# Optimization experiments

Hardware: AMD Instinct MI355X
Metric: run time of the kernel (lower is better)

The kernel has to match this reference:

```python
import jax, jax.numpy as jnp
import numpy as np

N_HEADS = 32
N_KV_HEADS = 8
HEAD_DIM = 128
DIM = 4096
BSZ = 2
SEQLEN = 2048
ROPE_THETA = 500000.0


def setup_inputs() -> dict:
    key = jax.random.key(0)
    ks = jax.random.split(key, 6)
    s = 0.02
    x = jax.random.normal(ks[0], (BSZ, SEQLEN, DIM), dtype=jnp.float32)
    wq = jax.random.normal(ks[1], (N_HEADS * HEAD_DIM, DIM), dtype=jnp.float32) * s
    wk = jax.random.normal(ks[2], (N_KV_HEADS * HEAD_DIM, DIM), dtype=jnp.float32) * s
    wv = jax.random.normal(ks[3], (N_KV_HEADS * HEAD_DIM, DIM), dtype=jnp.float32) * s
    wo = jax.random.normal(ks[4], (DIM, N_HEADS * HEAD_DIM), dtype=jnp.float32) * s
    cache_k = jnp.zeros((BSZ, SEQLEN, N_KV_HEADS, HEAD_DIM), dtype=jnp.float32)
    cache_v = jnp.zeros((BSZ, SEQLEN, N_KV_HEADS, HEAD_DIM), dtype=jnp.float32)
    # rotary frequencies: freqs_cis[t, j] = exp(i * t * theta^(-2j/hd)); pass cos/sin parts
    inv = 1.0 / (ROPE_THETA ** (jnp.arange(0, HEAD_DIM, 2, dtype=jnp.float32) / HEAD_DIM))
    t = jnp.arange(SEQLEN, dtype=jnp.float32)
    ang = jnp.outer(t, inv)  # [S, hd/2]
    freqs_cos = jnp.cos(ang)
    freqs_sin = jnp.sin(ang)
    # causal additive mask
    mask = jnp.triu(jnp.full((SEQLEN, SEQLEN), -jnp.inf, dtype=jnp.float32), k=1)
    return {"x": x, "wq": wq, "wk": wk, "wv": wv, "wo": wo,
            "cache_k": cache_k, "cache_v": cache_v,
            "freqs_cos": freqs_cos, "freqs_sin": freqs_sin,
            "mask": mask, "start_pos": 0}


def _apply_rope(t, cos, sin):
    # t: [B, S, h, hd]; cos/sin: [S, hd/2]
    B, S, h, hd = t.shape
    tf = t.astype(jnp.float32).reshape(B, S, h, hd // 2, 2)
    a, b = tf[..., 0], tf[..., 1]
    c = cos[None, :, None, :]
    s = sin[None, :, None, :]
    out = jnp.stack([a * c - b * s, a * s + b * c], axis=-1)
    return out.reshape(B, S, h, hd).astype(t.dtype)


def reference(x, wq, wk, wv, wo, cache_k, cache_v, freqs_cos, freqs_sin, mask, start_pos):
    B, S, D = x.shape
    hd = HEAD_DIM
    n_rep = N_HEADS // N_KV_HEADS
    xq = (x @ wq.T).reshape(B, S, N_HEADS, hd)
    xk = (x @ wk.T).reshape(B, S, N_KV_HEADS, hd)
    xv = (x @ wv.T).reshape(B, S, N_KV_HEADS, hd)
    xq = _apply_rope(xq, freqs_cos, freqs_sin)
    xk = _apply_rope(xk, freqs_cos, freqs_sin)
    # KV cache write + slice
    cache_k = jax.lax.dynamic_update_slice(cache_k, xk, (0, start_pos, 0, 0))
    cache_v = jax.lax.dynamic_update_slice(cache_v, xv, (0, start_pos, 0, 0))
    kv_len = start_pos + S
    keys = cache_k[:B, :kv_len]    # [B, K, kvh, hd]
    values = cache_v[:B, :kv_len]
    # GQA: repeat kv heads
    keys = jnp.repeat(keys, n_rep, axis=2)     # [B, K, H, hd]
    values = jnp.repeat(values, n_rep, axis=2)
    q = xq.transpose(0, 2, 1, 3)       # [B, H, S, hd]
    k = keys.transpose(0, 2, 1, 3)     # [B, H, K, hd]
    v = values.transpose(0, 2, 1, 3)
    scores = jnp.einsum('bhqd,bhkd->bhqk', q, k) / jnp.sqrt(jnp.float32(hd))
    if mask is not None:
        scores = scores + mask[None, None, :, :]
    probs = jax.nn.softmax(scores.astype(jnp.float32), axis=-1).astype(q.dtype)
    out = jnp.einsum('bhqk,bhkd->bhqd', probs, v)
    out = out.transpose(0, 2, 1, 3).reshape(B, S, N_HEADS * hd)
    return out @ wo.T
```

## Files before the change

### kernel.cpp

```cpp
#include <hip/hip_runtime.h>
#include <hip/hip_bf16.h>
#include <math.h>

typedef __attribute__((ext_vector_type(8)))  __bf16 bfrag;
typedef __attribute__((ext_vector_type(4)))  float  f32x4;
typedef __attribute__((ext_vector_type(16))) float  f32x16;
typedef __attribute__((ext_vector_type(8)))  short  s16x8;
typedef __attribute__((ext_vector_type(4)))  short  s16x4;
typedef __attribute__((ext_vector_type(2)))  unsigned u32x2;
typedef __attribute__((ext_vector_type(4)))  unsigned u32x4;

__device__ __forceinline__ short f2bf(float f) {
  return (short)__builtin_bit_cast(unsigned short, (__bf16)f);
}
__device__ __forceinline__ float bf2f(short s) {
  return (float)__builtin_bit_cast(__bf16, (unsigned short)s);
}
__device__ __forceinline__ unsigned cvtpk(float lo, float hi_) {
  unsigned r;
  asm("v_cvt_pk_bf16_f32 %0, %1, %2" : "=v"(r) : "v"(lo), "v"(hi_));
  return r;
}
__device__ __forceinline__ void gll16(const void* g, void* l) {
  __builtin_amdgcn_global_load_lds((const __attribute__((address_space(1))) void*)g,
                                   (__attribute__((address_space(3))) void*)l, 16, 0, 0);
}

__global__ __launch_bounds__(256) void cvt_f32_bf16(const float* __restrict__ in,
                                                    short* __restrict__ out, int n4) {
  int i = blockIdx.x * 256 + threadIdx.x;
  if (i >= n4) return;
  f32x4 v = ((const f32x4*)in)[i];
  s16x4 o;
  o.x = f2bf(v.x); o.y = f2bf(v.y); o.z = f2bf(v.z); o.w = f2bf(v.w);
  ((s16x4*)out)[i] = o;
}

__global__ __launch_bounds__(256) void cvt4(const float* __restrict__ x,
                                            const float* __restrict__ wq,
                                            const float* __restrict__ wk,
                                            const float* __restrict__ wv,
                                            short* __restrict__ xb,
                                            short* __restrict__ wqb,
                                            short* __restrict__ wkb,
                                            short* __restrict__ wvb) {
  const int b = blockIdx.x;
  const float* in; short* out; int base;
  if (b < 16384)      { in = x;  out = xb;  base = 0; }
  else if (b < 32768) { in = wq; out = wqb; base = 16384 * 256; }
  else if (b < 36864) { in = wk; out = wkb; base = 32768 * 256; }
  else                { in = wv; out = wvb; base = 36864 * 256; }
  const int idx = b * 256 + threadIdx.x - base;
  f32x4 v = ((const f32x4*)in)[idx];
  s16x4 o;
  o.x = f2bf(v.x); o.y = f2bf(v.y); o.z = f2bf(v.z); o.w = f2bf(v.w);
  ((s16x4*)out)[idx] = o;
}

template<bool BF16OUT>
__global__ __launch_bounds__(512) void gemm128n(const short* __restrict__ A,
                                                const short* __restrict__ B,
                                                void* __restrict__ Cv,
                                                int M, int N, int K, int NBX) {
  __shared__ __align__(16) short As[2][128 * 64];
  __shared__ __align__(16) short Bs[2][256 * 64];
  const int tid = threadIdx.x, lane = tid & 63, wid = tid >> 6;
  const int lr = lane & 15, lg = lane >> 4;
  const int wm = wid >> 2, wn = wid & 3;
  const int orig = blockIdx.x;
  const int xc = orig & 7, o8 = orig >> 3;
  const int s8 = o8 >> 5, t8 = o8 & 31;
  const int bmi = ((xc >> 1) << 3) + (t8 >> 2);
  const int bni = (xc & 1) * (NBX >> 1) + (s8 << 2) + (t8 & 3);
  const int bm = bmi << 7, bn = bni << 8;
  const int NT = K >> 6;
  const int r0 = tid >> 3;
  const int c0 = tid & 7;
  const int csrc = c0 ^ (r0 & 7);

#define STG(OP, OPs, boff, bb, hh, kt_)                                          \
  do {                                                                           \
    _Pragma("unroll")                                                            \
    for (int s = 0; s < 2; ++s)                                                  \
      gll16(OP + (size_t)(boff + (hh) * 128 + s * 64 + r0) * K + (kt_) * 64 + csrc * 8, \
            (char*)OPs[bb] + ((hh) * 128 + s * 64 + wid * 8) * 128);             \
  } while (0)

  int ch[2];
#pragma unroll
  for (int ks = 0; ks < 2; ++ks) ch[ks] = (((ks << 2) | lg) ^ (lr & 7)) << 4;
  const int aoff  = (wm * 64 + lr) * 128;
  const int boff2 = (wn * 32 + lr) * 128;

#define RD_A(dst, bb)                                                            \
  do {                                                                           \
    const char* ab = (const char*)As[bb] + aoff;                                 \
    _Pragma("unroll") for (int i = 0; i < 4; ++i)                                \
      _Pragma("unroll") for (int ks = 0; ks < 2; ++ks)                           \
        dst[i][ks] = *(const bfrag*)(ab + i * 2048 + ch[ks]);                    \
  } while (0)
#define RD_B(dst, bb, jh)                                                        \
  do {                                                                           \
    const char* bp = (const char*)Bs[bb] + boff2 + (jh) * 16384;                 \
    _Pragma("unroll") for (int j = 0; j < 2; ++j)                                \
      _Pragma("unroll") for (int ks = 0; ks < 2; ++ks)                           \
        dst[j][ks] = *(const bfrag*)(bp + j * 2048 + ch[ks]);                    \
  } while (0)
#define MFMA16(af, bf, jh)                                                       \
  do {                                                                           \
    __builtin_amdgcn_s_setprio(1);                                               \
    _Pragma("unroll") for (int ks = 0; ks < 2; ++ks)                             \
      _Pragma("unroll") for (int i = 0; i < 4; ++i)                              \
        _Pragma("unroll") for (int j = 0; j < 2; ++j)                            \
          acc[i][(jh) * 2 + j] = __builtin_amdgcn_mfma_f32_16x16x32_bf16(        \
              af[i][ks], bf[j][ks], acc[i][(jh) * 2 + j], 0, 0, 0);              \
    __builtin_amdgcn_s_setprio(0);                                               \
  } while (0)

  STG(A, As, bm, 0, 0, 0);
  STG(B, Bs, bn, 0, 0, 0);
  STG(B, Bs, bn, 0, 1, 0);
  if (NT > 1) {
    STG(A, As, bm, 1, 0, 1);
    STG(B, Bs, bn, 1, 0, 1);
    asm volatile("s_waitcnt vmcnt(4)" ::: "memory");
  } else {
    asm volatile("s_waitcnt vmcnt(0)" ::: "memory");
  }
  __builtin_amdgcn_s_barrier();
  __builtin_amdgcn_sched_barrier(0);

  f32x4 acc[4][4] = {};
  bfrag a_[4][2], b_lo[2][2], b_hi[2][2];

  for (int kt = 0; kt < NT; ++kt) {
    const int b = kt & 1;
    RD_A(a_, b);
    RD_B(b_lo, b, 0);
    if (kt + 1 < NT) STG(B, Bs, bn, b ^ 1, 1, kt + 1);
    MFMA16(a_, b_lo, 0);
    __builtin_amdgcn_s_barrier();
    __builtin_amdgcn_sched_barrier(0);
    RD_B(b_hi, b, 1);
    if (kt + 2 < NT) {
      STG(A, As, bm, b, 0, kt + 2);
      STG(B, Bs, bn, b, 0, kt + 2);
    }
    MFMA16(a_, b_hi, 1);
    if (kt + 1 < NT) {
      if (kt + 2 < NT) asm volatile("s_waitcnt vmcnt(4)" ::: "memory");
      else             asm volatile("s_waitcnt vmcnt(0)" ::: "memory");
      __builtin_amdgcn_s_barrier();
      __builtin_amdgcn_sched_barrier(0);
    }
  }
#undef STG
#undef RD_A
#undef RD_B
#undef MFMA16
  const int rb = bm + wm * 64 + lg * 4, cb = bn + wn * 32 + lr;
#pragma unroll
  for (int i = 0; i < 4; ++i)
#pragma unroll
    for (int jh = 0; jh < 2; ++jh)
#pragma unroll
      for (int j = 0; j < 2; ++j)
#pragma unroll
        for (int r = 0; r < 4; ++r) {
          size_t idx = (size_t)(rb + i * 16 + r) * N + (cb + jh * 128 + j * 16);
          if (BF16OUT) ((short*)Cv)[idx] = f2bf(acc[i][jh * 2 + j][r]);
          else         ((float*)Cv)[idx] = acc[i][jh * 2 + j][r];
        }
}

__global__ __launch_bounds__(256) void rope_k(short* __restrict__ qkv,
                                              const float* __restrict__ fcos,
                                              const float* __restrict__ fsin) {
  const int t = blockIdx.x;
  const int s = t & 2047;
  unsigned* row = (unsigned*)(qkv + (size_t)t * 6144);
  for (int p = threadIdx.x; p < 2560; p += 256) {
    const int h = p >> 6, i = p & 63;
    const int w = h * 64 + i;
    unsigned u = row[w];
    float a  = bf2f((short)(u & 0xffff));
    float b  = bf2f((short)(u >> 16));
    float c  = fcos[s * 64 + i], sn = fsin[s * 64 + i];
    float na = a * c - b * sn;
    float nb = a * sn + b * c;
    row[w] = ((unsigned)(unsigned short)f2bf(na)) |
             (((unsigned)(unsigned short)f2bf(nb)) << 16);
  }
}

__global__ __launch_bounds__(256) void vtrans(const short* __restrict__ qkv,
                                              short* __restrict__ vt) {
  const int sb = blockIdx.x, kvh = blockIdx.y, b = blockIdx.z;
  __shared__ short T[64][136];
  const int tid = threadIdx.x;
#pragma unroll
  for (int it = 0; it < 4; ++it) {
    int c = it * 256 + tid;
    int r = c >> 4, dc = c & 15;
    s16x8 v = *(const s16x8*)(qkv + (size_t)(b * 2048 + sb * 64 + r) * 6144
                              + 5120 + kvh * 128 + dc * 8);
    *(s16x8*)&T[r][dc * 8] = v;
  }
  __syncthreads();
#pragma unroll
  for (int it = 0; it < 4; ++it) {
    int c = it * 256 + tid;
    int d = c >> 3, sc = c & 7;
    s16x8 v;
#pragma unroll
    for (int j = 0; j < 8; ++j) v[j] = T[sc * 8 + j][d];
    *(s16x8*)(vt + (size_t)((b * 8 + kvh) * 128 + d) * 2048 + sb * 64 + sc * 8) = v;
  }
}

__global__ __launch_bounds__(512, 2) void fattn2(const short* __restrict__ qkv,
                                                 const short* __restrict__ vt,
                                                 short* __restrict__ ao) {
  const int b = blockIdx.z, h = blockIdx.y;
  const int qb = b ? (int)gridDim.x - 1 - blockIdx.x : blockIdx.x;
  const int kvh = h >> 2;
  const int tid = threadIdx.x;
  const int lane = tid & 63, wid = tid >> 6;
  const int l31 = lane & 31, hi = lane >> 5;
  __shared__ __align__(16) short Ks[2][64 * 128];
  __shared__ __align__(16) short Vs[2][128 * 64];

  const int q0w   = qb * 256 + wid * 32;
  const int qg    = q0w + l31;
  const int tmaxw = q0w >> 6;
  const int NT    = 4 * qb + 4;

  bfrag qf[8];
  {
    const short* qp = qkv + (size_t)(b * 2048 + qg) * 6144 + h * 128 + hi * 8;
#pragma unroll
    for (int kk = 0; kk < 8; ++kk) qf[kk] = *(const bfrag*)(qp + kk * 16);
  }

  const int kr0 = tid >> 4, kcc = tid & 15;
  const int vd0 = tid >> 3, vkc = tid & 7;
  const int kro[2] = { kr0, kr0 + 32 };
  const int vdo[2] = { vd0, vd0 + 64 };
  int kldst[2], vldst[2];
#pragma unroll
  for (int i = 0; i < 2; ++i) {
    kldst[i] = (kro[i] * 256 + kcc * 16) ^ ((kro[i] & 7) << 4);
    vldst[i] = (vdo[i] * 128 + vkc * 16) ^ ((vdo[i] & 7) << 4);
  }
  const short* base_k = qkv + (size_t)(b * 2048) * 6144 + 4096 + kvh * 128;
  const short* base_v = vt + (size_t)((b * 8 + kvh) * 128) * 2048;

  {
    s16x8 kr_[2], vr_[2];
#pragma unroll
    for (int i = 0; i < 2; ++i) {
      kr_[i] = *(const s16x8*)(base_k + (size_t)kro[i] * 6144 + kcc * 8);
      vr_[i] = *(const s16x8*)(base_v + (size_t)vdo[i] * 2048 + vkc * 8);
    }
#pragma unroll
    for (int i = 0; i < 2; ++i) {
      *(s16x8*)((char*)Ks[0] + kldst[i]) = kr_[i];
      *(s16x8*)((char*)Vs[0] + vldst[i]) = vr_[i];
    }
  }
  __syncthreads();

  f32x16 o[4] = {};
  float m = -3.0e38f, l = 0.f;
  const float c0 = 0.08838834764831845f * 1.4426950408889634f;
  const int  sw = (l31 & 7) << 4;

  for (int t = 0; t < NT; ++t) {
    const int cur = t & 1;
    s16x8 kr_[2], vr_[2];
    const bool pf = (t + 1 < NT);
    if (pf) {
#pragma unroll
      for (int i = 0; i < 2; ++i) {
        kr_[i] = *(const s16x8*)(base_k + (size_t)((t + 1) * 64 + kro[i]) * 6144 + kcc * 8);
        vr_[i] = *(const s16x8*)(base_v + (size_t)vdo[i] * 2048 + (t + 1) * 64 + vkc * 8);
      }
    }
    if (t <= tmaxw) {
      f32x16 st[2] = {};
      {
        const char* kb = (const char*)Ks[cur] + l31 * 256;
        __builtin_amdgcn_s_setprio(1);
#pragma unroll
        for (int kk = 0; kk < 8; ++kk) {
          const int ko = (kk * 32 + hi * 16) ^ sw;
          bfrag kf0 = *(const bfrag*)(kb + ko);
          bfrag kf1 = *(const bfrag*)(kb + 8192 + ko);
          st[0] = __builtin_amdgcn_mfma_f32_32x32x16_bf16(kf0, qf[kk], st[0], 0, 0, 0);
          st[1] = __builtin_amdgcn_mfma_f32_32x32x16_bf16(kf1, qf[kk], st[1], 0, 0, 0);
        }
        __builtin_amdgcn_s_setprio(0);
      }
      if (t == tmaxw) {
        const int kb0 = t * 64 + 4 * hi;
#pragma unroll
        for (int kt = 0; kt < 2; ++kt)
#pragma unroll
          for (int r = 0; r < 16; ++r) {
            int k = kb0 + kt * 32 + (r & 3) + 8 * (r >> 2);
            if (k > qg) st[kt][r] = -3.0e38f;
          }
      }
      float mt = -3.0e38f;
#pragma unroll
      for (int kt = 0; kt < 2; ++kt)
#pragma unroll
        for (int r = 0; r < 16; ++r) mt = fmaxf(mt, st[kt][r]);
      mt = fmaxf(mt, __shfl_xor(mt, 32, 64));
      if (!__all((mt - m) * c0 <= 8.0f)) {
        float nm = fmaxf(m, mt);
        float fe = exp2f((m - nm) * c0);
        m = nm;
        l *= fe;
#pragma unroll
        for (int dt = 0; dt < 4; ++dt)
#pragma unroll
          for (int r = 0; r < 16; ++r) o[dt][r] *= fe;
      }
      const float mc = m * c0;
      float ps = 0.f;
#pragma unroll
      for (int kt = 0; kt < 2; ++kt)
#pragma unroll
        for (int r = 0; r < 16; ++r) {
          float p = exp2f(st[kt][r] * c0 - mc);
          st[kt][r] = p;
          ps += p;
        }
      ps += __shfl_xor(ps, 32, 64);
      l += ps;
      bfrag pfr[4];
#pragma unroll
      for (int kt = 0; kt < 2; ++kt) {
        u32x2 a0 = __builtin_amdgcn_permlane32_swap(cvtpk(st[kt][0],  st[kt][1]),
                                                    cvtpk(st[kt][4],  st[kt][5]),  0, 0);
        u32x2 a1 = __builtin_amdgcn_permlane32_swap(cvtpk(st[kt][2],  st[kt][3]),
                                                    cvtpk(st[kt][6],  st[kt][7]),  0, 0);
        u32x2 b0 = __builtin_amdgcn_permlane32_swap(cvtpk(st[kt][8],  st[kt][9]),
                                                    cvtpk(st[kt][12], st[kt][13]), 0, 0);
        u32x2 b1 = __builtin_amdgcn_permlane32_swap(cvtpk(st[kt][10], st[kt][11]),
                                                    cvtpk(st[kt][14], st[kt][15]), 0, 0);
        u32x4 w0 = { a0.x, a1.x, a0.y, a1.y };
        u32x4 w1 = { b0.x, b1.x, b0.y, b1.y };
        pfr[kt * 2]     = __builtin_bit_cast(bfrag, w0);
        pfr[kt * 2 + 1] = __builtin_bit_cast(bfrag, w1);
      }
      __builtin_amdgcn_s_setprio(1);
#pragma unroll
      for (int ks = 0; ks < 4; ++ks) {
        const char* vb = (const char*)Vs[cur] + l31 * 128 + ((ks * 32 + hi * 16) ^ sw);
#pragma unroll
        for (int dt = 0; dt < 4; ++dt) {
          bfrag vf = *(const bfrag*)(vb + dt * 4096);
          o[dt] = __builtin_amdgcn_mfma_f32_32x32x16_bf16(vf, pfr[ks], o[dt], 0, 0, 0);
        }
      }
      __builtin_amdgcn_s_setprio(0);
    }
    __syncthreads();
    if (pf) {
#pragma unroll
      for (int i = 0; i < 2; ++i) {
        *(s16x8*)((char*)Ks[cur ^ 1] + kldst[i]) = kr_[i];
        *(s16x8*)((char*)Vs[cur ^ 1] + vldst[i]) = vr_[i];
      }
    }
    __syncthreads();
  }
  const float linv = 1.f / l;
  short* aop = ao + (size_t)(b * 2048 + qg) * 4096 + h * 128 + 4 * hi;
#pragma unroll
  for (int dt = 0; dt < 4; ++dt)
#pragma unroll
    for (int r = 0; r < 16; ++r) {
      int d = dt * 32 + (r & 3) + 8 * (r >> 2);
      aop[d] = f2bf(o[dt][r] * linv);
    }
}

extern "C" void kernel_launch(void* const* d_in, const int* in_sizes, int n_in,
                              void* d_out, int out_size, void* d_ws, size_t ws_size,
                              hipStream_t stream) {
  const float* x  = (const float*)d_in[0];
  const float* wq = (const float*)d_in[1];
  const float* wk = (const float*)d_in[2];
  const float* wv = (const float*)d_in[3];
  const float* wo = (const float*)d_in[4];
  const float* fc = (const float*)d_in[7];
  const float* fs = (const float*)d_in[8];

  char* ws = (char*)d_ws;
  short* xb    = (short*)(ws);
  short* ao    = xb;
  short* wqkvb = (short*)(ws + 33554432ull);
  short* qkv   = (short*)(ws + 83886080ull);
  short* vt    = (short*)(ws + 134217728ull);
  short* wob   = (short*)(ws + 167772160ull);

  cvt4<<<40960, 256, 0, stream>>>(x, wq, wk, wv,
                                  xb, wqkvb, wqkvb + 16777216, wqkvb + 20971520);
  gemm128n<true ><<<768, 512, 0, stream>>>(xb, wqkvb, qkv, 4096, 6144, 4096, 24);
  rope_k<<<4096, 256, 0, stream>>>(qkv, fc, fs);
  vtrans<<<dim3(32, 8, 2), 256, 0, stream>>>(qkv, vt);
  cvt_f32_bf16<<<16384, 256, 0, stream>>>(wo, wob, 4194304);
  fattn2<<<dim3(8, 32, 2), 512, 0, stream>>>(qkv, vt, ao);
  gemm128n<false><<<512, 512, 0, stream>>>(ao, wob, (float*)d_out, 4096, 4096, 4096, 16);
}
```

Measured before the change: 504.5 us.

## Use 256x256 tiled ping-pong GEMM kernel for output projection

Adds a new GEMM kernel that computes 256x256 output tiles per 512-thread block, with 8 waves each owning a 128x64 sub-tile. Global-to-LDS loads are interleaved with quarter-tile MFMA phases across a two-buffer pipeline. The output projection now launches 256 blocks instead of 512. The goal is better operand reuse and fewer LDS and global loads per FLOP, at the cost of more accumulator registers, 128KB of LDS, and only 256 blocks to spread over the GPU's CUs.

```diff
diff --git a/kernel.cpp b/kernel.cpp
--- a/kernel.cpp
+++ b/kernel.cpp
@@ -56,6 +56,14 @@
   o.x = f2bf(v.x); o.y = f2bf(v.y); o.z = f2bf(v.z); o.w = f2bf(v.w);
   ((s16x4*)out)[idx] = o;
 }
+
+#define STG_(OP, OPs, boff, bb, hh, kt_, Kd)                                     \
+  do {                                                                           \
+    _Pragma("unroll")                                                            \
+    for (int s = 0; s < 2; ++s)                                                  \
+      gll16(OP + (size_t)(boff + (hh) * 128 + s * 64 + r0) * Kd + (kt_) * 64 + csrc * 8, \
+            (char*)OPs[bb] + ((hh) * 128 + s * 64 + wid * 8) * 128);             \
+  } while (0)
 
 template<bool BF16OUT>
 __global__ __launch_bounds__(512) void gemm128n(const short* __restrict__ A,
@@ -78,14 +86,6 @@
   const int c0 = tid & 7;
   const int csrc = c0 ^ (r0 & 7);
 
-#define STG(OP, OPs, boff, bb, hh, kt_)                                          \
-  do {                                                                           \
-    _Pragma("unroll")                                                            \
-    for (int s = 0; s < 2; ++s)                                                  \
-      gll16(OP + (size_t)(boff + (hh) * 128 + s * 64 + r0) * K + (kt_) * 64 + csrc * 8, \
-            (char*)OPs[bb] + ((hh) * 128 + s * 64 + wid * 8) * 128);             \
-  } while (0)
-
   int ch[2];
 #pragma unroll
   for (int ks = 0; ks < 2; ++ks) ch[ks] = (((ks << 2) | lg) ^ (lr & 7)) << 4;
@@ -117,12 +117,12 @@
     __builtin_amdgcn_s_setprio(0);                                               \
   } while (0)
 
-  STG(A, As, bm, 0, 0, 0);
-  STG(B, Bs, bn, 0, 0, 0);
-  STG(B, Bs, bn, 0, 1, 0);
+  STG_(A, As, bm, 0, 0, 0, K);
+  STG_(B, Bs, bn, 0, 0, 0, K);
+  STG_(B, Bs, bn, 0, 1, 0, K);
   if (NT > 1) {
-    STG(A, As, bm, 1, 0, 1);
-    STG(B, Bs, bn, 1, 0, 1);
+    STG_(A, As, bm, 1, 0, 1, K);
+    STG_(B, Bs, bn, 1, 0, 1, K);
     asm volatile("s_waitcnt vmcnt(4)" ::: "memory");
   } else {
     asm volatile("s_waitcnt vmcnt(0)" ::: "memory");
@@ -137,14 +137,14 @@
     const int b = kt & 1;
     RD_A(a_, b);
     RD_B(b_lo, b, 0);
-    if (kt + 1 < NT) STG(B, Bs, bn, b ^ 1, 1, kt + 1);
+    if (kt + 1 < NT) STG_(B, Bs, bn, b ^ 1, 1, kt + 1, K);
     MFMA16(a_, b_lo, 0);
     __builtin_amdgcn_s_barrier();
     __builtin_amdgcn_sched_barrier(0);
     RD_B(b_hi, b, 1);
     if (kt + 2 < NT) {
-      STG(A, As, bm, b, 0, kt + 2);
-      STG(B, Bs, bn, b, 0, kt + 2);
+      STG_(A, As, bm, b, 0, kt + 2, K);
+      STG_(B, Bs, bn, b, 0, kt + 2, K);
     }
     MFMA16(a_, b_hi, 1);
     if (kt + 1 < NT) {
@@ -154,7 +154,6 @@
       __builtin_amdgcn_sched_barrier(0);
     }
   }
-#undef STG
 #undef RD_A
 #undef RD_B
 #undef MFMA16
@@ -171,6 +170,138 @@
           if (BF16OUT) ((short*)Cv)[idx] = f2bf(acc[i][jh * 2 + j][r]);
           else         ((float*)Cv)[idx] = acc[i][jh * 2 + j][r];
         }
+}
+
+template<bool BF16OUT>
+__global__ __launch_bounds__(512) void gemm256p(const short* __restrict__ A,
+                                                const short* __restrict__ B,
+                                                void* __restrict__ Cv,
+                                                int M, int N, int K, int NBX) {
+  __shared__ __align__(16) short As[2][256 * 64];
+  __shared__ __align__(16) short Bs[2][256 * 64];
+  const int tid = threadIdx.x, lane = tid & 63, wid = tid >> 6;
+  const int lr = lane & 15, lg = lane >> 4;
+  const int wm = wid >> 2, wn = wid & 3;
+  const int orig = blockIdx.x;
+  const int xc = orig & 7, o8 = orig >> 3;
+  const int bmi = ((xc >> 1) << 2) + (o8 & 3);
+  const int bni = (xc & 1) * (NBX >> 1) + (o8 >> 2);
+  const int bm = bmi << 8, bn = bni << 8;
+  const int NT = K >> 6;
+  const int r0 = tid >> 3;
+  const int c0 = tid & 7;
+  const int csrc = c0 ^ (r0 & 7);
+
+  int ch[2];
+#pragma unroll
+  for (int ks = 0; ks < 2; ++ks) ch[ks] = (((ks << 2) | lg) ^ (lr & 7)) << 4;
+  const int aoff = (wm * 128 + lr) * 128;
+  const int boff = (wn * 64 + lr) * 128;
+
+#define RD_A8(dst, bb, ih)                                                       \
+  do {                                                                           \
+    const char* ab = (const char*)As[bb] + aoff + (ih) * 8192;                   \
+    _Pragma("unroll") for (int i = 0; i < 4; ++i)                                \
+      _Pragma("unroll") for (int ks = 0; ks < 2; ++ks)                           \
+        dst[i][ks] = *(const bfrag*)(ab + i * 2048 + ch[ks]);                    \
+  } while (0)
+#define RD_B4(dst, bb, jh)                                                       \
+  do {                                                                           \
+    const char* bp = (const char*)Bs[bb] + boff + (jh) * 4096;                   \
+    _Pragma("unroll") for (int j = 0; j < 2; ++j)                                \
+      _Pragma("unroll") for (int ks = 0; ks < 2; ++ks)                           \
+        dst[j][ks] = *(const bfrag*)(bp + j * 2048 + ch[ks]);                    \
+  } while (0)
+#define QUAD(af, bf, ih, jh)                                                     \
+  do {                                                                           \
+    __builtin_amdgcn_s_setprio(1);                                               \
+    _Pragma("unroll") for (int ks = 0; ks < 2; ++ks)                             \
+      _Pragma("unroll") for (int i = 0; i < 4; ++i)                              \
+        _Pragma("unroll") for (int j = 0; j < 2; ++j)                            \
+          acc[(ih) * 4 + i][(jh) * 2 + j] = __builtin_amdgcn_mfma_f32_16x16x32_bf16( \
+              af[i][ks], bf[j][ks], acc[(ih) * 4 + i][(jh) * 2 + j], 0, 0, 0);   \
+    __builtin_amdgcn_s_setprio(0);                                               \
+  } while (0)
+#define BARRIER() do { __builtin_amdgcn_s_barrier(); __builtin_amdgcn_sched_barrier(0); } while (0)
+
+  STG_(A, As, bm, 0, 0, 0, K); STG_(A, As, bm, 0, 1, 0, K);
+  STG_(B, Bs, bn, 0, 0, 0, K); STG_(B, Bs, bn, 0, 1, 0, K);
+  STG_(B, Bs, bn, 1, 0, 1, K); STG_(B, Bs, bn, 1, 1, 1, K);
+  asm volatile("s_waitcnt vmcnt(4)" ::: "memory");
+  BARRIER();
+
+  f32x4 acc[8][4] = {};
+  bfrag a_[4][2], b_lo[2][2], b_hi[2][2];
+  const int NI = NT >> 1;
+
+  for (int it = 0; it < NI; ++it) {
+    const int O  = 2 * it + 1;
+    int E2 = 2 * it + 2; if (E2 >= NT) E2 = 0;
+    int O2 = 2 * it + 3; if (O2 >= NT) O2 = 0;
+    RD_A8(a_, 0, 0);
+    RD_B4(b_lo, 0, 0);
+    STG_(A, As, bm, 1, 0, O, K);
+    BARRIER();
+    asm volatile("s_waitcnt lgkmcnt(0)" ::: "memory");
+    QUAD(a_, b_lo, 0, 0);
+    BARRIER();
+    RD_B4(b_hi, 0, 1);
+    STG_(A, As, bm, 1, 1, O, K);
+    BARRIER();
+    asm volatile("s_waitcnt lgkmcnt(0)" ::: "memory");
+    QUAD(a_, b_hi, 0, 1);
+    BARRIER();
+    RD_A8(a_, 0, 1);
+    STG_(B, Bs, bn, 0, 0, E2, K);
+    BARRIER();
+    asm volatile("s_waitcnt lgkmcnt(0)" ::: "memory");
+    QUAD(a_, b_hi, 1, 1);
+    BARRIER();
+    STG_(B, Bs, bn, 0, 1, E2, K);
+    asm volatile("s_waitcnt vmcnt(4)" ::: "memory");
+    BARRIER();
+    QUAD(a_, b_lo, 1, 0);
+    BARRIER();
+    RD_A8(a_, 1, 0);
+    RD_B4(b_lo, 1, 0);
+    STG_(A, As, bm, 0, 0, E2, K);
+    BARRIER();
+    asm volatile("s_waitcnt lgkmcnt(0)" ::: "memory");
+    QUAD(a_, b_lo, 0, 0);
+    BARRIER();
+    RD_B4(b_hi, 1, 1);
+    STG_(A, As, bm, 0, 1, E2, K);
+    BARRIER();
+    asm volatile("s_waitcnt lgkmcnt(0)" ::: "memory");
+    QUAD(a_, b_hi, 0, 1);
+    BARRIER();
+    RD_A8(a_, 1, 1);
+    STG_(B, Bs, bn, 1, 0, O2, K);
+    BARRIER();
+    asm volatile("s_waitcnt lgkmcnt(0)" ::: "memory");
+    QUAD(a_, b_hi, 1, 1);
+    BARRIER();
+    STG_(B, Bs, bn, 1, 1, O2, K);
+    asm volatile("s_waitcnt vmcnt(4)" ::: "memory");
+    BARRIER();
+    QUAD(a_, b_lo, 1, 0);
+    BARRIER();
+  }
+#undef RD_A8
+#undef RD_B4
+#undef QUAD
+#undef BARRIER
+  const int rb = bm + wm * 128 + lg * 4, cb = bn + wn * 64 + lr;
+#pragma unroll
+  for (int i = 0; i < 8; ++i)
+#pragma unroll
+    for (int j = 0; j < 4; ++j)
+#pragma unroll
+      for (int r = 0; r < 4; ++r) {
+        size_t idx = (size_t)(rb + i * 16 + r) * N + (cb + j * 16);
+        if (BF16OUT) ((short*)Cv)[idx] = f2bf(acc[i][j][r]);
+        else         ((float*)Cv)[idx] = acc[i][j][r];
+      }
 }
 
 __global__ __launch_bounds__(256) void rope_k(short* __restrict__ qkv,
@@ -414,5 +545,5 @@
   vtrans<<<dim3(32, 8, 2), 256, 0, stream>>>(qkv, vt);
   cvt_f32_bf16<<<16384, 256, 0, stream>>>(wo, wob, 4194304);
   fattn2<<<dim3(8, 32, 2), 512, 0, stream>>>(qkv, vt, ao);
-  gemm128n<false><<<512, 512, 0, stream>>>(ao, wob, (float*)d_out, 4096, 4096, 4096, 16);
-}
+  gemm256p<false><<<256, 512, 0, stream>>>(ao, wob, (float*)d_out, 4096, 4096, 4096, 16);
+}
```

Result: faster. 491.9 us (-2.5%).
